# Kernel optimization log

Measured on AMD Instinct MI355X. Metric: run time of the kernel, lower is better.

Reference implementation:

```python
import jax, jax.numpy as jnp
import numpy as np
from jax import lax

N_ITERS = 3
NUM_CAPS_IN = 768   # 32 * 4 * 6
NUM_CAPS_OUT = 64
CAPS_DIM_IN = 8
CAPS_DIM_OUT = 16


def _conv2d(x, w, b, stride):
    # x: NCHW, w: OIHW, VALID padding
    y = lax.conv_general_dilated(x, w, (stride, stride), 'VALID',
                                 dimension_numbers=('NCHW', 'OIHW', 'NCHW'))
    return y + b[None, :, None, None]


def _squash(x, axis):
    # norm**2 / (1 + norm**2) * x / norm  (as in the torch source)
    norm = jnp.linalg.norm(x, axis=axis, keepdims=True)
    return (norm ** 2) / (1.0 + norm ** 2) * x / norm


def setup_inputs() -> dict:
    key = jax.random.key(0)
    ks = jax.random.split(key, 4)
    B = 128
    x = jax.random.normal(ks[0], (B, 3, 32, 42), dtype=jnp.float32)
    conv1_w = jax.random.normal(ks[1], (32, 3, 6, 6), dtype=jnp.float32) * 0.1
    conv1_b = jnp.zeros((32,), dtype=jnp.float32)
    pc_w = jax.random.normal(ks[2], (256, 32, 3, 3), dtype=jnp.float32) * 0.1
    pc_b = jnp.zeros((256,), dtype=jnp.float32)
    # FinalCapsule W: (num_caps_in, num_caps_out, caps_dim_out, caps_dim_in)
    route_w = jax.random.normal(ks[3], (NUM_CAPS_IN, NUM_CAPS_OUT, CAPS_DIM_OUT, CAPS_DIM_IN), dtype=jnp.float32)
    return {"x": x, "conv1_w": conv1_w, "conv1_b": conv1_b,
            "pc_w": pc_w, "pc_b": pc_b, "route_w": route_w}


def reference(x, conv1_w, conv1_b, pc_w, pc_b, route_w):
    B = x.shape[0]
    # conv1: k=6, s=3 -> (B,32,9,13)
    h = jax.nn.relu(_conv2d(x, conv1_w, conv1_b, 3))
    # primary capsules: k=3, s=2 -> (B,256,4,6) -> (B,768,8)
    h = _conv2d(h, pc_w, pc_b, 2)
    u = h.reshape(B, -1, CAPS_DIM_IN)
    u = _squash(u, axis=-1)
    # prediction vectors: W[i,o,:,:] @ u[b,i,:] -> xh (B, 768, 64, 16)
    xh = jnp.einsum('iokd,bid->biok', route_w, u)
    xhd = lax.stop_gradient(xh)
    b_logits = jnp.zeros((B, NUM_CAPS_IN, NUM_CAPS_OUT), dtype=xh.dtype)
    for _ in range(N_ITERS - 1):
        c = jax.nn.softmax(b_logits, axis=2)                      # (B,768,64)
        s = jnp.sum(c[..., None] * xhd, axis=1, keepdims=True)   # (B,1,64,16)
        v = _squash(s, axis=-1)
        b_logits = b_logits + jnp.sum(xhd * v, axis=-1)
    c = jax.nn.softmax(b_logits, axis=2)
    s = jnp.sum(c[..., None] * xh, axis=1, keepdims=True)
    v = _squash(s, axis=-1)                                       # (B,1,64,16)
    return v[:, 0].reshape(B, NUM_CAPS_OUT * CAPS_DIM_OUT)        # (B,1024)
```

## Files before the change

### kernel.cpp

```cpp
#include <hip/hip_runtime.h>
#include <math.h>

#define BATCH 128
#define NCI 768
#define NCO 64
#define DIN 8
#define DOUT 16

typedef __attribute__((ext_vector_type(8))) short bfrag;
typedef __attribute__((ext_vector_type(4))) float f32x4;
typedef __attribute__((ext_vector_type(16))) float f32x16;

__device__ __forceinline__ void split8(const float* x, bfrag& hi, bfrag& lo) {
    #pragma unroll
    for (int j = 0; j < 8; ++j) {
        unsigned xb = __float_as_uint(x[j]);
        unsigned hb = xb & 0xffff0000u;
        float lf = x[j] - __uint_as_float(hb);
        hi[j] = (short)(xb >> 16);
        lo[j] = (short)(__float_as_uint(lf) >> 16);
    }
}

__global__ __launch_bounds__(256) void conv1_kernel(
    const float* __restrict__ x, const float* __restrict__ w,
    const float* __restrict__ bias, float* __restrict__ h1) {
    __shared__ float wl[32 * 3 * 36];
    for (int i = threadIdx.x; i < 3456; i += 256) wl[i] = w[i];
    __syncthreads();
    int idx = blockIdx.x * 256 + threadIdx.x;
    const int total = BATCH * 32 * 9 * 13;
    if (idx >= total) return;
    int ow = idx % 13; int t = idx / 13;
    int oh = t % 9; t /= 9;
    int oc = t % 32; int b = t / 32;
    float acc = bias[oc];
    const float* xb = x + (size_t)b * 3 * 32 * 42;
    #pragma unroll
    for (int ic = 0; ic < 3; ++ic) {
        const float* xc = xb + ic * 32 * 42 + (oh * 3) * 42 + ow * 3;
        const float* wc = wl + (oc * 3 + ic) * 36;
        #pragma unroll
        for (int kh = 0; kh < 6; ++kh)
            #pragma unroll
            for (int kw = 0; kw < 6; ++kw)
                acc += xc[kh * 42 + kw] * wc[kh * 6 + kw];
    }
    h1[idx] = fmaxf(acc, 0.f);
}

__global__ __launch_bounds__(256) void im2col_kernel(
    const float* __restrict__ h1, float* __restrict__ B2) {
    int idx = blockIdx.x * 256 + threadIdx.x;
    if (idx >= 36 * 3072) return;
    int n = idx % 3072, ko = idx / 3072;
    int b = n / 24, s = n % 24, h = s / 6, w = s % 6;
    const float* hb = h1 + (size_t)b * 3744 + (2 * h) * 13 + 2 * w;
    float out[8];
    #pragma unroll
    for (int j = 0; j < 8; ++j) {
        int k = ko * 8 + j;
        int ic = k / 9, r = k % 9;
        int kh = r / 3, kw = r % 3;
        out[j] = hb[ic * 117 + kh * 13 + kw];
    }
    *(float4*)(B2 + (size_t)idx * 8) = *(const float4*)out;
    *(float4*)(B2 + (size_t)idx * 8 + 4) = *(const float4*)(out + 4);
}

__global__ __launch_bounds__(256) void pc_gemm_kernel(
    const float* __restrict__ wpc, const float* __restrict__ bias,
    const float* __restrict__ B2, float* __restrict__ u2) {
    int wv = threadIdx.x >> 6;
    int l = threadIdx.x & 63;
    int q = l >> 4, r16 = l & 15;
    int c2t = blockIdx.y * 4 + wv;
    int n0 = blockIdx.x * 16;
    f32x4 acc = {0.f, 0.f, 0.f, 0.f};
    int c2a = c2t * 16 + r16;
    const float* ap0 = wpc + (size_t)c2a * 288 + q * 8;
    const float* bp0 = B2 + ((size_t)q * 3072 + n0 + r16) * 8;
    #pragma unroll
    for (int ks = 0; ks < 9; ++ks) {
        float av[8], bv[8];
        *(float4*)av = *(const float4*)(ap0 + ks * 32);
        *(float4*)(av + 4) = *(const float4*)(ap0 + ks * 32 + 4);
        *(float4*)bv = *(const float4*)(bp0 + (size_t)ks * 4 * 3072 * 8);
        *(float4*)(bv + 4) = *(const float4*)(bp0 + (size_t)ks * 4 * 3072 * 8 + 4);
        bfrag ahi, alo, bhi, blo;
        split8(av, ahi, alo);
        split8(bv, bhi, blo);
        acc = __builtin_amdgcn_mfma_f32_16x16x32_bf16(ahi, bhi, acc, 0, 0, 0);
        acc = __builtin_amdgcn_mfma_f32_16x16x32_bf16(ahi, blo, acc, 0, 0, 0);
        acc = __builtin_amdgcn_mfma_f32_16x16x32_bf16(alo, bhi, acc, 0, 0, 0);
    }
    int n = n0 + r16;
    int b = n / 24, s = n % 24;
    float vals[4], n2[4];
    #pragma unroll
    for (int r = 0; r < 4; ++r) {
        float xv = acc[r] + bias[c2t * 16 + q * 4 + r];
        vals[r] = xv;
        n2[r] = xv * xv;
    }
    #pragma unroll
    for (int r = 0; r < 4; ++r) {
        n2[r] += __shfl_xor(n2[r], 1, 64);
        n2[r] += __shfl_xor(n2[r], 2, 64);
        n2[r] += __shfl_xor(n2[r], 4, 64);
    }
    #pragma unroll
    for (int r = 0; r < 4; ++r) {
        int c2 = c2t * 16 + q * 4 + r;
        int cap = c2 * 3 + (s >> 3);
        int d = s & 7;
        float nr = sqrtf(n2[r]);
        u2[((size_t)(cap * 2 + (d >> 2)) * 128 + b) * 4 + (d & 3)]
            = vals[r] * nr / (1.f + n2[r]);
    }
}

__global__ __launch_bounds__(128) void mz_kernel(
    const float* __restrict__ blog, float* __restrict__ m_, float* __restrict__ z_) {
    int i = blockIdx.x;
    int b = threadIdx.x;
    const float* src = blog + (size_t)i * 128 + b;
    float r[64];
    float m = -1e30f;
    #pragma unroll
    for (int o = 0; o < 64; ++o) {
        r[o] = src[(size_t)o * 98304];
        m = fmaxf(m, r[o]);
    }
    float sum = 0.f;
    #pragma unroll
    for (int o = 0; o < 64; ++o) sum += __expf(r[o] - m);
    m_[i * 128 + b] = m;
    z_[i * 128 + b] = 1.f / sum;
}

template <bool UNIFORM>
__global__ __launch_bounds__(256, 4) void spass_kernel(
    const float* __restrict__ W, const float* __restrict__ u2,
    const float* __restrict__ blog, const float* __restrict__ m_,
    const float* __restrict__ z_, float* __restrict__ s_part) {
    int o = blockIdx.x;
    int it = blockIdx.y;
    int wv = threadIdx.x >> 6;
    int l = threadIdx.x & 63;
    int q = l >> 4, r16 = l & 15;
    int i0 = it * 32;
    f32x4 acc0 = {0.f, 0.f, 0.f, 0.f};
    f32x4 acc1 = {0.f, 0.f, 0.f, 0.f};

    float4 w0[2], w1[2];
    float4 ua[2][2][2];
    float bl[2][2], mv[2][2], zv[2][2];

    auto issue = [&](int s, int buf) {
        int cap = i0 + s * 4 + q;
        const float* wp = W + ((size_t)cap * 64 + o) * 128 + r16 * 8;
        w0[buf] = *(const float4*)wp;
        w1[buf] = *(const float4*)(wp + 4);
        #pragma unroll
        for (int m = 0; m < 2; ++m) {
            int b = wv * 32 + m * 16 + r16;
            ua[buf][m][0] = *(const float4*)(u2 + ((size_t)(cap * 2 + 0) * 128 + b) * 4);
            ua[buf][m][1] = *(const float4*)(u2 + ((size_t)(cap * 2 + 1) * 128 + b) * 4);
            if (!UNIFORM) {
                bl[buf][m] = blog[((size_t)o * 768 + cap) * 128 + b];
                mv[buf][m] = m_[cap * 128 + b];
                zv[buf][m] = z_[cap * 128 + b];
            }
        }
    };

    issue(0, 0);
    #pragma unroll
    for (int s = 0; s < 8; ++s) {
        int cur = s & 1, nxt = cur ^ 1;
        if (s < 7) issue(s + 1, nxt);
        float wv8[8];
        *(float4*)(wv8) = w0[cur];
        *(float4*)(wv8 + 4) = w1[cur];
        bfrag bhi, blo;
        split8(wv8, bhi, blo);
        #pragma unroll
        for (int m = 0; m < 2; ++m) {
            float uv[8];
            *(float4*)(uv) = ua[cur][m][0];
            *(float4*)(uv + 4) = ua[cur][m][1];
            if (!UNIFORM) {
                float c = __expf(bl[cur][m] - mv[cur][m]) * zv[cur][m];
                #pragma unroll
                for (int j = 0; j < 8; ++j) uv[j] *= c;
            }
            bfrag ahi, alo;
            split8(uv, ahi, alo);
            if (m == 0) {
                acc0 = __builtin_amdgcn_mfma_f32_16x16x32_bf16(ahi, bhi, acc0, 0, 0, 0);
                acc0 = __builtin_amdgcn_mfma_f32_16x16x32_bf16(ahi, blo, acc0, 0, 0, 0);
                acc0 = __builtin_amdgcn_mfma_f32_16x16x32_bf16(alo, bhi, acc0, 0, 0, 0);
            } else {
                acc1 = __builtin_amdgcn_mfma_f32_16x16x32_bf16(ahi, bhi, acc1, 0, 0, 0);
                acc1 = __builtin_amdgcn_mfma_f32_16x16x32_bf16(ahi, blo, acc1, 0, 0, 0);
                acc1 = __builtin_amdgcn_mfma_f32_16x16x32_bf16(alo, bhi, acc1, 0, 0, 0);
            }
        }
    }
    #pragma unroll
    for (int reg = 0; reg < 4; ++reg) {
        int b0 = wv * 32 + q * 4 + reg;
        s_part[(((size_t)it * 128 + b0) * 64 + o) * 16 + r16] = acc0[reg];
        int b1 = b0 + 16;
        s_part[(((size_t)it * 128 + b1) * 64 + o) * 16 + r16] = acc1[reg];
    }
}

template <bool TRANSPOSED>
__global__ __launch_bounds__(256) void squashv_kernel(
    const float* __restrict__ s_part, float* __restrict__ v, float scale) {
    int idx = blockIdx.x * 256 + threadIdx.x;
    float acc = 0.f;
    #pragma unroll
    for (int it = 0; it < 24; ++it) acc += s_part[(size_t)it * 131072 + idx];
    acc *= scale;
    float n2 = acc * acc;
    n2 += __shfl_xor(n2, 1, 64);
    n2 += __shfl_xor(n2, 2, 64);
    n2 += __shfl_xor(n2, 4, 64);
    n2 += __shfl_xor(n2, 8, 64);
    float n = sqrtf(n2);
    float val = acc * n / (1.f + n2);
    if (TRANSPOSED) {
        int k = idx & 15, o = (idx >> 4) & 63, b = idx >> 10;
        v[((size_t)o * 128 + b) * 16 + k] = val;
    } else {
        v[idx] = val;
    }
}

template <bool ACCUM>
__global__ __launch_bounds__(256, 4) void bpass_kernel(
    const float* __restrict__ W, const float* __restrict__ u2,
    const float* __restrict__ v_t, float* __restrict__ blog) {
    int o = blockIdx.x, it = blockIdx.y;
    int tid = threadIdx.x;
    int wv = tid >> 6;
    int l = tid & 63;
    int r = l & 31;
    int kh = l >> 5;
    int capB = it * 32;
    __shared__ float wl[32 * 164];
    #pragma unroll
    for (int itr = 0; itr < 4; ++itr) {
        int F = tid + 256 * itr;
        int cap = F >> 5, slot = F & 31;
        int k = slot >> 1, dh = slot & 1;
        float4 t4 = *(const float4*)(W + ((size_t)(capB + cap) * 64 + o) * 128 + k * 8 + dh * 4);
        float* dst = wl + cap * 164 + (dh * 4) * 20 + k;
        dst[0] = t4.x; dst[20] = t4.y; dst[40] = t4.z; dst[60] = t4.w;
    }
    bfrag vhi[4], vlo[4];
    #pragma unroll
    for (int nt = 0; nt < 4; ++nt) {
        const float* vp = v_t + ((size_t)o * 128 + nt * 32 + r) * 16 + kh * 8;
        float vv8[8];
        *(float4*)(vv8) = *(const float4*)vp;
        *(float4*)(vv8 + 4) = *(const float4*)(vp + 4);
        split8(vv8, vhi[nt], vlo[nt]);
    }
    __syncthreads();
    #pragma unroll
    for (int mt = 0; mt < 2; ++mt) {
        int cl = wv * 8 + mt * 4 + (r >> 3);
        const float* ap = wl + cl * 164 + (r & 7) * 20 + kh * 8;
        float a8[8];
        *(float4*)(a8) = *(const float4*)ap;
        *(float4*)(a8 + 4) = *(const float4*)(ap + 4);
        int capg = capB + wv * 8 + mt * 4;
        int gw = kh * 2;
        float4 u4[4][4];
        #pragma unroll
        for (int nt = 0; nt < 4; ++nt) {
            int b = nt * 32 + r;
            #pragma unroll
            for (int g = 0; g < 4; ++g)
                u4[nt][g] = *(const float4*)(u2 + ((size_t)((capg + g) * 2 + kh) * 128 + b) * 4);
        }
        float prevv[4][2];
        if (ACCUM) {
            #pragma unroll
            for (int nt = 0; nt < 4; ++nt) {
                int b = nt * 32 + r;
                #pragma unroll
                for (int gg = 0; gg < 2; ++gg)
                    prevv[nt][gg] = blog[((size_t)o * 768 + capg + gw + gg) * 128 + b];
            }
        }
        bfrag ahi, alo;
        split8(a8, ahi, alo);
        #pragma unroll
        for (int nt = 0; nt < 4; ++nt) {
            int b = nt * 32 + r;
            f32x16 acc;
            #pragma unroll
            for (int z = 0; z < 16; ++z) acc[z] = 0.f;
            acc = __builtin_amdgcn_mfma_f32_32x32x16_bf16(ahi, vhi[nt], acc, 0, 0, 0);
            acc = __builtin_amdgcn_mfma_f32_32x32x16_bf16(ahi, vlo[nt], acc, 0, 0, 0);
            acc = __builtin_amdgcn_mfma_f32_32x32x16_bf16(alo, vhi[nt], acc, 0, 0, 0);
            float full[4];
            #pragma unroll
            for (int g = 0; g < 4; ++g) {
                float part = u4[nt][g].x * acc[g * 4 + 0] + u4[nt][g].y * acc[g * 4 + 1]
                           + u4[nt][g].z * acc[g * 4 + 2] + u4[nt][g].w * acc[g * 4 + 3];
                full[g] = part + __shfl_xor(part, 32, 64);
            }
            #pragma unroll
            for (int gg = 0; gg < 2; ++gg) {
                int g = gw + gg;
                size_t bi = ((size_t)o * 768 + capg + g) * 128 + b;
                blog[bi] = (ACCUM ? prevv[nt][gg] : 0.f) + full[g];
            }
        }
    }
}

extern "C" void kernel_launch(void* const* d_in, const int* in_sizes, int n_in,
                              void* d_out, int out_size, void* d_ws, size_t ws_size,
                              hipStream_t stream) {
    const float* x  = (const float*)d_in[0];
    const float* w1 = (const float*)d_in[1];
    const float* b1 = (const float*)d_in[2];
    const float* wp = (const float*)d_in[3];
    const float* bp = (const float*)d_in[4];
    const float* W  = (const float*)d_in[5];
    float* out = (float*)d_out;
    float* ws = (float*)d_ws;

    float* u2     = ws;
    float* blog   = ws + 786432;
    float* m_     = ws + 7077888;
    float* z_     = ws + 7176192;
    float* v      = ws + 7274496;
    float* s_part = ws + 7405568;
    float* B2     = s_part;
    float* h1     = s_part + 884736;

    conv1_kernel<<<1872, 256, 0, stream>>>(x, w1, b1, h1);
    im2col_kernel<<<432, 256, 0, stream>>>(h1, B2);
    pc_gemm_kernel<<<dim3(192, 4), 256, 0, stream>>>(wp, bp, B2, u2);

    spass_kernel<true><<<dim3(64, 24), 256, 0, stream>>>(W, u2, nullptr, nullptr, nullptr, s_part);
    squashv_kernel<true><<<512, 256, 0, stream>>>(s_part, v, 1.f / 64.f);
    bpass_kernel<false><<<dim3(64, 24), 256, 0, stream>>>(W, u2, v, blog);

    mz_kernel<<<768, 128, 0, stream>>>(blog, m_, z_);
    spass_kernel<false><<<dim3(64, 24), 256, 0, stream>>>(W, u2, blog, m_, z_, s_part);
    squashv_kernel<true><<<512, 256, 0, stream>>>(s_part, v, 1.f);
    bpass_kernel<true><<<dim3(64, 24), 256, 0, stream>>>(W, u2, v, blog);

    mz_kernel<<<768, 128, 0, stream>>>(blog, m_, z_);
    spass_kernel<false><<<dim3(64, 24), 256, 0, stream>>>(W, u2, blog, m_, z_, s_part);
    squashv_kernel<false><<<512, 256, 0, stream>>>(s_part, out, 1.f);
}
```

Baseline: 162.6 us.

## Stage route weights in LDS, deepen prefetch, double-buffer u loads in blog pass

The s-pass kernel now loads each block's 32-capsule slice of W cooperatively into shared memory with coalesced float4 loads, then reads the weight fragments from LDS instead of issuing per-lane global loads inside the loop. The u/logit prefetch goes from double- to triple-buffered so loads are issued two steps ahead. The logit-update kernel replaces one up-front batch of 16 float4 u loads with a two-slot rolling prefetch to lower register pressure. In exchange the s-pass uses about 17KB of LDS, adds a barrier, and holds more prefetched registers, which may reduce occupancy.

```diff
diff --git a/kernel.cpp b/kernel.cpp
--- a/kernel.cpp
+++ b/kernel.cpp
@@ -146,22 +146,17 @@
     const float* __restrict__ z_, float* __restrict__ s_part) {
     int o = blockIdx.x;
     int it = blockIdx.y;
-    int wv = threadIdx.x >> 6;
-    int l = threadIdx.x & 63;
+    int tid = threadIdx.x;
+    int wv = tid >> 6;
+    int l = tid & 63;
     int q = l >> 4, r16 = l & 15;
     int i0 = it * 32;
-    f32x4 acc0 = {0.f, 0.f, 0.f, 0.f};
-    f32x4 acc1 = {0.f, 0.f, 0.f, 0.f};
-
-    float4 w0[2], w1[2];
-    float4 ua[2][2][2];
-    float bl[2][2], mv[2][2], zv[2][2];
-
+    __shared__ float wl[32 * 132];
+
+    float4 ua[3][2][2];
+    float bl[3][2], mv[3][2], zv[3][2];
     auto issue = [&](int s, int buf) {
         int cap = i0 + s * 4 + q;
-        const float* wp = W + ((size_t)cap * 64 + o) * 128 + r16 * 8;
-        w0[buf] = *(const float4*)wp;
-        w1[buf] = *(const float4*)(wp + 4);
         #pragma unroll
         for (int m = 0; m < 2; ++m) {
             int b = wv * 32 + m * 16 + r16;
@@ -176,13 +171,26 @@
     };
 
     issue(0, 0);
+    issue(1, 1);
+    #pragma unroll
+    for (int itr = 0; itr < 4; ++itr) {
+        int F = tid + 256 * itr;
+        int cap = F >> 5, slot = F & 31;
+        float4 t4 = *(const float4*)(W + ((size_t)(i0 + cap) * 64 + o) * 128 + slot * 4);
+        *(float4*)(wl + cap * 132 + slot * 4) = t4;
+    }
+    __syncthreads();
+
+    f32x4 acc0 = {0.f, 0.f, 0.f, 0.f};
+    f32x4 acc1 = {0.f, 0.f, 0.f, 0.f};
     #pragma unroll
     for (int s = 0; s < 8; ++s) {
-        int cur = s & 1, nxt = cur ^ 1;
-        if (s < 7) issue(s + 1, nxt);
+        int cur = s % 3;
+        if (s < 6) issue(s + 2, (s + 2) % 3);
+        const float* wp = wl + (s * 4 + q) * 132 + r16 * 8;
         float wv8[8];
-        *(float4*)(wv8) = w0[cur];
-        *(float4*)(wv8 + 4) = w1[cur];
+        *(float4*)(wv8) = *(const float4*)wp;
+        *(float4*)(wv8 + 4) = *(const float4*)(wp + 4);
         bfrag bhi, blo;
         split8(wv8, bhi, blo);
         #pragma unroll
@@ -280,14 +288,6 @@
         *(float4*)(a8 + 4) = *(const float4*)(ap + 4);
         int capg = capB + wv * 8 + mt * 4;
         int gw = kh * 2;
-        float4 u4[4][4];
-        #pragma unroll
-        for (int nt = 0; nt < 4; ++nt) {
-            int b = nt * 32 + r;
-            #pragma unroll
-            for (int g = 0; g < 4; ++g)
-                u4[nt][g] = *(const float4*)(u2 + ((size_t)((capg + g) * 2 + kh) * 128 + b) * 4);
-        }
         float prevv[4][2];
         if (ACCUM) {
             #pragma unroll
@@ -298,10 +298,21 @@
                     prevv[nt][gg] = blog[((size_t)o * 768 + capg + gw + gg) * 128 + b];
             }
         }
+        float4 u4b[2][4];
+        #pragma unroll
+        for (int g = 0; g < 4; ++g)
+            u4b[0][g] = *(const float4*)(u2 + ((size_t)((capg + g) * 2 + kh) * 128 + r) * 4);
         bfrag ahi, alo;
         split8(a8, ahi, alo);
         #pragma unroll
         for (int nt = 0; nt < 4; ++nt) {
+            int cur = nt & 1;
+            if (nt < 3) {
+                int bn = (nt + 1) * 32 + r;
+                #pragma unroll
+                for (int g = 0; g < 4; ++g)
+                    u4b[cur ^ 1][g] = *(const float4*)(u2 + ((size_t)((capg + g) * 2 + kh) * 128 + bn) * 4);
+            }
             int b = nt * 32 + r;
             f32x16 acc;
             #pragma unroll
@@ -312,8 +323,8 @@
             float full[4];
             #pragma unroll
             for (int g = 0; g < 4; ++g) {
-                float part = u4[nt][g].x * acc[g * 4 + 0] + u4[nt][g].y * acc[g * 4 + 1]
-                           + u4[nt][g].z * acc[g * 4 + 2] + u4[nt][g].w * acc[g * 4 + 3];
+                float part = u4b[cur][g].x * acc[g * 4 + 0] + u4b[cur][g].y * acc[g * 4 + 1]
+                           + u4b[cur][g].z * acc[g * 4 + 2] + u4b[cur][g].w * acc[g * 4 + 3];
                 full[g] = part + __shfl_xor(part, 32, 64);
             }
             #pragma unroll
```

New measurement: 160.6 us. Within noise of the previous version (-1.2%).
